# Kernel optimization log

Hardware: AMD Instinct MI355X
Metric: run time of the kernel (lower is better)

Reference implementation:

```python
import jax, jax.numpy as jnp
import numpy as np
import math

B, L, D = 4, 512, 768
H, DH, R = 12, 64, 128


def _layernorm(x, g, b, eps=1e-5):
    mu = jnp.mean(x, axis=-1, keepdims=True)
    var = jnp.var(x, axis=-1, keepdims=True)
    return (x - mu) * jax.lax.rsqrt(var + eps) * g + b


def setup_inputs() -> dict:
    key = jax.random.key(0)
    ks = jax.random.split(key, 8)
    s = 0.02
    return {
        "x": jax.random.normal(ks[0], (B, L, D), jnp.float32),
        "W_qkv": jax.random.normal(ks[1], (D, 3 * D), jnp.float32) * s,
        "b_qkv": jnp.zeros((3 * D,), jnp.float32),
        "W_b1": jax.random.normal(ks[2], (D, R), jnp.float32) * s,
        "W_b2": jax.random.normal(ks[3], (R, H * 5), jnp.float32) * s,
        "temperature": jnp.ones((1,), jnp.float32) * 0.5,
        "W_proj": jax.random.normal(ks[4], (D, D), jnp.float32) * s,
        "b_proj": jnp.zeros((D,), jnp.float32),
        "ln_g": jnp.ones((D,), jnp.float32),
        "ln_b": jnp.zeros((D,), jnp.float32),
        "mem_g": jnp.ones((DH,), jnp.float32),
        "mem_b": jnp.zeros((DH,), jnp.float32),
    }


def reference(x, W_qkv, b_qkv, W_b1, W_b2, temperature, W_proj, b_proj, ln_g, ln_b, mem_g, mem_b):
    Bq, Lq, Dq = x.shape
    xn = _layernorm(x, ln_g, ln_b)
    qkv = xn @ W_qkv + b_qkv
    q, k, v = jnp.split(qkv, 3, axis=-1)

    # bottleneck gating params: (B, L, H, 5)
    params = (jax.nn.silu(x @ W_b1) @ W_b2).reshape(Bq, Lq, H, 5)
    sem_amp = jax.nn.sigmoid(params[..., 0])
    sem_phase = jnp.tanh(params[..., 1]) * math.pi
    ctx_amp = jax.nn.sigmoid(params[..., 2])
    ctx_phase = jnp.tanh(params[..., 3]) * math.pi
    decay = 0.5 + 0.49 * jax.nn.sigmoid(params[..., 4])  # (B,L,H)

    temp = jnp.clip(temperature, 0.1, 2.0)  # (1,) broadcasts
    interference = jnp.tanh(sem_amp * ctx_amp * jnp.cos(sem_phase - ctx_phase)) * temp
    gate = jax.nn.sigmoid(interference)  # (B,L,H)

    qf = (jax.nn.elu(q) + 1.0).reshape(Bq, Lq, H, DH)
    kf = (jax.nn.elu(k) + 1.0).reshape(Bq, Lq, H, DH)
    vf = v.reshape(Bq, Lq, H, DH)

    log_decay = jnp.log(decay + 1e-8)
    cld = jnp.maximum(jnp.cumsum(log_decay, axis=1), -85.0)  # (B,L,H)
    df = jnp.exp(cld)
    inv_df = jnp.exp(-cld)
    ema = 1.0 - decay  # (B,L,H)

    # kv outer products gated by interference: (B,L,H,DH,DH)
    kv_all = jnp.einsum('blhd,blhe->blhde', kf, vf) * (1.0 + gate)[..., None, None]
    kv_states = jnp.cumsum(kv_all * (ema * inv_df)[..., None, None], axis=1) * df[..., None, None]

    z_states = jnp.cumsum(kf * (ema * inv_df)[..., None], axis=1) * df[..., None]  # (B,L,H,DH)

    out_num = jnp.einsum('blhd,blhde->blhe', qf, kv_states)
    den = jnp.sum(qf * z_states, axis=-1, keepdims=True) + 1e-6
    out = out_num / den  # (B,L,H,DH)

    out = _layernorm(out, mem_g, mem_b)
    attn_out = out.reshape(Bq, Lq, Dq)
    return attn_out @ W_proj + b_proj, gate
```

## Files before the change

### kernel.cpp

```cpp
#include <hip/hip_runtime.h>
#include <math.h>

#define PI_F 3.14159265358979323846f

static constexpr int L_ = 512, D_ = 768, H_ = 12, DH_ = 64;
static constexpr int BL_ = 2048;
static constexpr int BLD_ = BL_ * D_;
static constexpr int NC_ = 8;
static constexpr int BH_ = 48;

__global__ void sentinel_kernel(float* out, float code, float aux) {
  out[0] = code; out[1] = aux;
}

__global__ __launch_bounds__(256) void ln_kernel(const float* __restrict__ x,
                                                 const float* __restrict__ g,
                                                 const float* __restrict__ b,
                                                 float* __restrict__ xn) {
  int row = blockIdx.x, tid = threadIdx.x;
  const float* xr = x + (size_t)row * D_;
  float v0 = xr[tid], v1 = xr[tid + 256], v2 = xr[tid + 512];
  float s = v0 + v1 + v2;
  float s2 = v0 * v0 + v1 * v1 + v2 * v2;
#pragma unroll
  for (int off = 32; off > 0; off >>= 1) { s += __shfl_xor(s, off); s2 += __shfl_xor(s2, off); }
  __shared__ float red[8];
  if ((tid & 63) == 0) { red[tid >> 6] = s; red[4 + (tid >> 6)] = s2; }
  __syncthreads();
  float st = red[0] + red[1] + red[2] + red[3];
  float qt = red[4] + red[5] + red[6] + red[7];
  float mu = st * (1.0f / D_);
  float var = qt * (1.0f / D_) - mu * mu;
  float rs = rsqrtf(var + 1e-5f);
  float* xo = xn + (size_t)row * D_;
  xo[tid]       = (v0 - mu) * rs * g[tid]       + b[tid];
  xo[tid + 256] = (v1 - mu) * rs * g[tid + 256] + b[tid + 256];
  xo[tid + 512] = (v2 - mu) * rs * g[tid + 512] + b[tid + 512];
}

template <int MODE>
__global__ __launch_bounds__(256) void gemm_fast(const float* __restrict__ A,
                                                 const float* __restrict__ Bm,
                                                 const float* __restrict__ bias,
                                                 float* __restrict__ O0,
                                                 float* __restrict__ O1,
                                                 float* __restrict__ O2,
                                                 int N, int K) {
  __shared__ float As[16][68];
  __shared__ float Bs[16][68];
  int tid = threadIdx.x;
  int tx = tid & 15, ty = tid >> 4;
  int row0 = blockIdx.y * 64, col0 = blockIdx.x * 64;
  float acc[4][4] = {};
  int ar = tid >> 2, ak = (tid & 3) * 4;
  int bk = tid >> 4, bc = (tid & 15) * 4;
  for (int k0 = 0; k0 < K; k0 += 16) {
    float4 a4 = *(const float4*)&A[(size_t)(row0 + ar) * K + k0 + ak];
    As[ak + 0][ar] = a4.x; As[ak + 1][ar] = a4.y;
    As[ak + 2][ar] = a4.z; As[ak + 3][ar] = a4.w;
    *(float4*)&Bs[bk][bc] = *(const float4*)&Bm[(size_t)(k0 + bk) * N + col0 + bc];
    __syncthreads();
#pragma unroll
    for (int kk = 0; kk < 16; ++kk) {
      float4 av = *(float4*)&As[kk][ty * 4];
      float4 bv = *(float4*)&Bs[kk][tx * 4];
      acc[0][0] += av.x * bv.x; acc[0][1] += av.x * bv.y; acc[0][2] += av.x * bv.z; acc[0][3] += av.x * bv.w;
      acc[1][0] += av.y * bv.x; acc[1][1] += av.y * bv.y; acc[1][2] += av.y * bv.z; acc[1][3] += av.y * bv.w;
      acc[2][0] += av.z * bv.x; acc[2][1] += av.z * bv.y; acc[2][2] += av.z * bv.z; acc[2][3] += av.z * bv.w;
      acc[3][0] += av.w * bv.x; acc[3][1] += av.w * bv.y; acc[3][2] += av.w * bv.z; acc[3][3] += av.w * bv.w;
    }
    __syncthreads();
  }
  if (MODE == 0) {
    int sec = col0 / 768;
    float* O = (sec == 0) ? O0 : ((sec == 1) ? O1 : O2);
    int lc = col0 - sec * 768 + tx * 4;
    float b0 = bias[col0 + tx * 4 + 0], b1 = bias[col0 + tx * 4 + 1];
    float b2 = bias[col0 + tx * 4 + 2], b3 = bias[col0 + tx * 4 + 3];
#pragma unroll
    for (int ii = 0; ii < 4; ++ii) {
      int r = row0 + ty * 4 + ii;
      float4 v;
      v.x = acc[ii][0] + b0; v.y = acc[ii][1] + b1;
      v.z = acc[ii][2] + b2; v.w = acc[ii][3] + b3;
      if (sec < 2) {
        v.x = (v.x > 0.f) ? v.x + 1.f : expf(v.x);
        v.y = (v.y > 0.f) ? v.y + 1.f : expf(v.y);
        v.z = (v.z > 0.f) ? v.z + 1.f : expf(v.z);
        v.w = (v.w > 0.f) ? v.w + 1.f : expf(v.w);
      }
      *(float4*)&O[(size_t)r * 768 + lc] = v;
    }
  } else if (MODE == 1) {
#pragma unroll
    for (int ii = 0; ii < 4; ++ii) {
      int r = row0 + ty * 4 + ii;
      float4 v;
      v.x = acc[ii][0]; v.y = acc[ii][1]; v.z = acc[ii][2]; v.w = acc[ii][3];
      v.x = v.x / (1.f + expf(-v.x));
      v.y = v.y / (1.f + expf(-v.y));
      v.z = v.z / (1.f + expf(-v.z));
      v.w = v.w / (1.f + expf(-v.w));
      *(float4*)&O0[(size_t)r * N + col0 + tx * 4] = v;
    }
  } else {
    float b0 = bias[col0 + tx * 4 + 0], b1 = bias[col0 + tx * 4 + 1];
    float b2 = bias[col0 + tx * 4 + 2], b3 = bias[col0 + tx * 4 + 3];
#pragma unroll
    for (int ii = 0; ii < 4; ++ii) {
      int r = row0 + ty * 4 + ii;
      float4 v;
      v.x = acc[ii][0] + b0; v.y = acc[ii][1] + b1;
      v.z = acc[ii][2] + b2; v.w = acc[ii][3] + b3;
      *(float4*)&O0[(size_t)r * N + col0 + tx * 4] = v;
    }
  }
}

__global__ __launch_bounds__(64) void params_kernel(const float* __restrict__ h1,
                                                    const float* __restrict__ Wb2,
                                                    const float* __restrict__ temp_p,
                                                    float* __restrict__ gate_out,
                                                    float* __restrict__ cg,
                                                    float* __restrict__ ce,
                                                    float* __restrict__ ld) {
  int t = blockIdx.x;
  int tid = threadIdx.x;
  __shared__ float hs[128];
  __shared__ float ps[60];
  *(float2*)&hs[tid * 2] = *(const float2*)&h1[(size_t)t * 128 + tid * 2];
  __syncthreads();
  if (tid < 60) {
    float acc = 0.f;
#pragma unroll 4
    for (int k = 0; k < 128; ++k) acc += hs[k] * Wb2[k * 60 + tid];
    ps[tid] = acc;
  }
  __syncthreads();
  if (tid < 12) {
    float p0 = ps[tid * 5 + 0], p1 = ps[tid * 5 + 1], p2 = ps[tid * 5 + 2];
    float p3 = ps[tid * 5 + 3], p4 = ps[tid * 5 + 4];
    float sa = 1.f / (1.f + expf(-p0));
    float sp = tanhf(p1) * PI_F;
    float ca = 1.f / (1.f + expf(-p2));
    float cp = tanhf(p3) * PI_F;
    float dec = 0.5f + 0.49f / (1.f + expf(-p4));
    float tmp = fminf(fmaxf(temp_p[0], 0.1f), 2.0f);
    float inter = tanhf(sa * ca * cosf(sp - cp)) * tmp;
    float gate = 1.f / (1.f + expf(-inter));
    gate_out[t * 12 + tid] = gate;
    int b = t >> 9, l = t & 511;
    int bhl = (b * 12 + tid) * L_ + l;
    float ema = 1.f - dec;
    cg[bhl] = ema * (1.f + gate);
    ce[bhl] = ema;
    ld[bhl] = logf(dec + 1e-8f);
  }
}

__global__ __launch_bounds__(64) void cld_kernel(const float* __restrict__ ld,
                                                 float* __restrict__ cld,
                                                 float* __restrict__ cEnd) {
  int bh = blockIdx.x;
  int lane = threadIdx.x;
  const float* src = ld + (size_t)bh * L_;
  float v[8];
  float s = 0.f;
#pragma unroll
  for (int i = 0; i < 8; ++i) { v[i] = src[lane * 8 + i]; s += v[i]; }
  float tot = s;
#pragma unroll
  for (int off = 1; off < 64; off <<= 1) {
    float n = __shfl_up(tot, off);
    if (lane >= off) tot += n;
  }
  float run = tot - s;
  float out7 = 0.f;
#pragma unroll
  for (int i = 0; i < 8; ++i) {
    run += v[i];
    float o = fmaxf(run, -85.f);
    cld[(size_t)bh * L_ + lane * 8 + i] = o;
    out7 = o;
  }
  if ((lane & 7) == 7) cEnd[bh * NC_ + (lane >> 3)] = out7;
}

__global__ __launch_bounds__(64) void infscan_kernel(const float* __restrict__ kf,
                                                     const float* __restrict__ ce,
                                                     const float* __restrict__ cld,
                                                     int* __restrict__ tstar) {
  int bh = blockIdx.x;
  int b = bh / H_, h = bh - b * H_;
  int e = threadIdx.x;
  float cz = 0.f;
  int tf = L_;
  for (int t = 0; t < L_; ++t) {
    int idx = bh * L_ + t;
    float s = ce[idx] * expf(-cld[idx]);
    float kv = kf[(size_t)(b * L_ + t) * D_ + h * DH_ + e];
    cz = cz + kv * s;
    if (tf == L_ && isinf(cz)) tf = t;
  }
#pragma unroll
  for (int off = 1; off < 64; off <<= 1) tf = min(tf, __shfl_xor(tf, off));
  if (e == 0) tstar[bh] = tf;
}

__global__ __launch_bounds__(256) void chunk_sum_kernel(const float* __restrict__ kf,
                                                        const float* __restrict__ vf,
                                                        const float* __restrict__ cg,
                                                        const float* __restrict__ ce,
                                                        const float* __restrict__ cld,
                                                        const float* __restrict__ cEnd,
                                                        float* __restrict__ T,
                                                        float* __restrict__ zc) {
  int blk = blockIdx.x;
  int c = blk & 7, bh = blk >> 3;
  int b = bh / H_, h = bh - b * H_;
  int tid = threadIdx.x;
  __shared__ float kfs[64][68];
  __shared__ float vfs[64][68];
  __shared__ float wv[64], wz[64];
  float cend = cEnd[blk];
  if (tid < 64) {
    int idx = bh * L_ + c * 64 + tid;
    float w = expf(cend - cld[idx]);
    wv[tid] = cg[idx] * w;
    wz[tid] = ce[idx] * w;
  }
  __syncthreads();
  int t = tid >> 2, g4 = (tid & 3) * 16;
  size_t rowb = (size_t)(b * L_ + c * 64 + t) * D_ + h * 64 + g4;
  float wvt = wv[t];
#pragma unroll
  for (int i = 0; i < 4; ++i) {
    *(float4*)&kfs[t][g4 + 4 * i] = *(const float4*)&kf[rowb + 4 * i];
    float4 vv = *(const float4*)&vf[rowb + 4 * i];
    vv.x *= wvt; vv.y *= wvt; vv.z *= wvt; vv.w *= wvt;
    *(float4*)&vfs[t][g4 + 4 * i] = vv;
  }
  __syncthreads();
  int d = tid >> 2, eb = (tid & 3) * 16;
  float4 a0 = {}, a1 = {}, a2 = {}, a3 = {};
  for (int tt = 0; tt < 64; ++tt) {
    float kd = kfs[tt][d];
    float4 x0 = *(float4*)&vfs[tt][eb + 0];
    float4 x1 = *(float4*)&vfs[tt][eb + 4];
    float4 x2 = *(float4*)&vfs[tt][eb + 8];
    float4 x3 = *(float4*)&vfs[tt][eb + 12];
    a0.x += kd * x0.x; a0.y += kd * x0.y; a0.z += kd * x0.z; a0.w += kd * x0.w;
    a1.x += kd * x1.x; a1.y += kd * x1.y; a1.z += kd * x1.z; a1.w += kd * x1.w;
    a2.x += kd * x2.x; a2.y += kd * x2.y; a2.z += kd * x2.z; a2.w += kd * x2.w;
    a3.x += kd * x3.x; a3.y += kd * x3.y; a3.z += kd * x3.z; a3.w += kd * x3.w;
  }
  size_t tb = (size_t)blk * 4096 + (size_t)d * 64 + eb;
  *(float4*)&T[tb + 0] = a0;
  *(float4*)&T[tb + 4] = a1;
  *(float4*)&T[tb + 8] = a2;
  *(float4*)&T[tb + 12] = a3;
  if (tid < 64) {
    float za = 0.f;
#pragma unroll 8
    for (int tt = 0; tt < 64; ++tt) za += kfs[tt][tid] * wz[tt];
    zc[blk * 64 + tid] = za;
  }
}

__global__ __launch_bounds__(256) void scan_kernel(float* __restrict__ T,
                                                   const float* __restrict__ zc,
                                                   const float* __restrict__ cEnd,
                                                   float* __restrict__ zprev) {
  int bh = blockIdx.x, tid = threadIdx.x;
  float4 s0 = {}, s1 = {}, s2 = {}, s3 = {};
  float zs = 0.f;
  float prevEnd = 0.f;
  for (int c = 0; c < NC_; ++c) {
    int blk = bh * NC_ + c;
    float r = expf(cEnd[blk] - prevEnd);
    prevEnd = cEnd[blk];
    size_t base = (size_t)blk * 4096 + (size_t)tid * 16;
    float4 t0 = *(const float4*)&T[base + 0];
    float4 t1 = *(const float4*)&T[base + 4];
    float4 t2 = *(const float4*)&T[base + 8];
    float4 t3 = *(const float4*)&T[base + 12];
    *(float4*)&T[base + 0] = s0;
    *(float4*)&T[base + 4] = s1;
    *(float4*)&T[base + 8] = s2;
    *(float4*)&T[base + 12] = s3;
    s0.x = s0.x * r + t0.x; s0.y = s0.y * r + t0.y; s0.z = s0.z * r + t0.z; s0.w = s0.w * r + t0.w;
    s1.x = s1.x * r + t1.x; s1.y = s1.y * r + t1.y; s1.z = s1.z * r + t1.z; s1.w = s1.w * r + t1.w;
    s2.x = s2.x * r + t2.x; s2.y = s2.y * r + t2.y; s2.z = s2.z * r + t2.z; s2.w = s2.w * r + t2.w;
    s3.x = s3.x * r + t3.x; s3.y = s3.y * r + t3.y; s3.z = s3.z * r + t3.z; s3.w = s3.w * r + t3.w;
    if (tid < 64) {
      zprev[blk * 64 + tid] = zs;
      zs = zs * r + zc[blk * 64 + tid];
    }
  }
}

__global__ __launch_bounds__(256) void chunk_out_kernel(const float* __restrict__ qf,
                                                        const float* __restrict__ kf,
                                                        const float* __restrict__ vf,
                                                        const float* __restrict__ cg,
                                                        const float* __restrict__ ce,
                                                        const float* __restrict__ cld,
                                                        const float* __restrict__ cEnd,
                                                        const float* __restrict__ Sprev,
                                                        const float* __restrict__ zprev,
                                                        const int* __restrict__ tstar,
                                                        const float* __restrict__ mg,
                                                        const float* __restrict__ mb,
                                                        float* __restrict__ attn) {
  int blk = blockIdx.x;
  int c = blk & 7, bh = blk >> 3;
  int b = bh / H_, h = bh - b * H_;
  int tid = threadIdx.x;
  __shared__ float qfs[64][68];
  __shared__ float kfs[64][68];
  __shared__ float vfs[64][68];
  __shared__ float cldS[64], cgS[64], ceS[64], zS[64];
  int t = tid >> 2, g4 = (tid & 3) * 16;
  size_t rowb = (size_t)(b * L_ + c * 64 + t) * D_ + h * 64 + g4;
#pragma unroll
  for (int i = 0; i < 4; ++i) {
    *(float4*)&qfs[t][g4 + 4 * i] = *(const float4*)&qf[rowb + 4 * i];
    *(float4*)&kfs[t][g4 + 4 * i] = *(const float4*)&kf[rowb + 4 * i];
    *(float4*)&vfs[t][g4 + 4 * i] = *(const float4*)&vf[rowb + 4 * i];
  }
  if (tid < 64) {
    int idx = bh * L_ + c * 64 + tid;
    cldS[tid] = cld[idx];
    cgS[tid] = cg[idx];
    ceS[tid] = ce[idx];
    zS[tid] = zprev[blk * 64 + tid];
  }
  __syncthreads();
  float prevEnd = (c == 0) ? 0.f : cEnd[blk - 1];
  int ts = tstar[bh];
  int i = tid >> 2, jb = (tid & 3) * 16;
  float sc[16];
#pragma unroll
  for (int jj = 0; jj < 16; ++jj) sc[jj] = 0.f;
  for (int d = 0; d < 64; d += 4) {
    float4 q4 = *(float4*)&qfs[i][d];
#pragma unroll
    for (int jj = 0; jj < 16; ++jj) {
      float4 k4 = *(float4*)&kfs[jb + jj][d];
      sc[jj] += q4.x * k4.x + q4.y * k4.y + q4.z * k4.z + q4.w * k4.w;
    }
  }
  float cldi = cldS[i];
  float den = 0.f;
  float mvals[16];
#pragma unroll
  for (int jj = 0; jj < 16; ++jj) {
    int j = jb + jj;
    float w = (j <= i) ? expf(cldi - cldS[j]) : 0.f;
    float sw = sc[jj] * w;
    den += sw * ceS[j];
    mvals[jj] = sw * cgS[j];
  }
  float dz = 0.f;
#pragma unroll
  for (int dd = 0; dd < 16; ++dd) dz += qfs[i][jb + dd] * zS[jb + dd];
  den += __shfl_xor(den, 1); den += __shfl_xor(den, 2);
  dz += __shfl_xor(dz, 1);  dz += __shfl_xor(dz, 2);
  float wi = expf(cldi - prevEnd);
  den += wi * dz + 1e-6f;
  __syncthreads();
#pragma unroll
  for (int jj = 0; jj < 16; ++jj) kfs[i][jb + jj] = mvals[jj];
  __syncthreads();
  float4 o0 = {}, o1 = {}, o2 = {}, o3 = {};
  for (int j = 0; j < 64; ++j) {
    float m = kfs[i][j];
    float4 x0 = *(float4*)&vfs[j][jb + 0];
    float4 x1 = *(float4*)&vfs[j][jb + 4];
    float4 x2 = *(float4*)&vfs[j][jb + 8];
    float4 x3 = *(float4*)&vfs[j][jb + 12];
    o0.x += m * x0.x; o0.y += m * x0.y; o0.z += m * x0.z; o0.w += m * x0.w;
    o1.x += m * x1.x; o1.y += m * x1.y; o1.z += m * x1.z; o1.w += m * x1.w;
    o2.x += m * x2.x; o2.y += m * x2.y; o2.z += m * x2.z; o2.w += m * x2.w;
    o3.x += m * x3.x; o3.y += m * x3.y; o3.z += m * x3.z; o3.w += m * x3.w;
  }
  float4 p0 = {}, p1 = {}, p2 = {}, p3 = {};
  size_t sb = (size_t)blk * 4096;
  for (int d = 0; d < 64; ++d) {
    float qd = qfs[i][d];
    float4 x0 = *(const float4*)&Sprev[sb + d * 64 + jb + 0];
    float4 x1 = *(const float4*)&Sprev[sb + d * 64 + jb + 4];
    float4 x2 = *(const float4*)&Sprev[sb + d * 64 + jb + 8];
    float4 x3 = *(const float4*)&Sprev[sb + d * 64 + jb + 12];
    p0.x += qd * x0.x; p0.y += qd * x0.y; p0.z += qd * x0.z; p0.w += qd * x0.w;
    p1.x += qd * x1.x; p1.y += qd * x1.y; p1.z += qd * x1.z; p1.w += qd * x1.w;
    p2.x += qd * x2.x; p2.y += qd * x2.y; p2.z += qd * x2.z; p2.w += qd * x2.w;
    p3.x += qd * x3.x; p3.y += qd * x3.y; p3.z += qd * x3.z; p3.w += qd * x3.w;
  }
  size_t ob = (size_t)(b * L_ + c * 64 + i) * D_ + h * 64 + jb;
  if (c * 64 + i >= ts) {
#pragma unroll
    for (int q4i = 0; q4i < 4; ++q4i) {
      float4 w4;
      w4.x = mb[jb + q4i * 4 + 0]; w4.y = mb[jb + q4i * 4 + 1];
      w4.z = mb[jb + q4i * 4 + 2]; w4.w = mb[jb + q4i * 4 + 3];
      *(float4*)&attn[ob + q4i * 4] = w4;
    }
    return;
  }
  float inv = 1.0f / den;
  float o[16];
  o[0] = (o0.x + wi * p0.x) * inv;  o[1] = (o0.y + wi * p0.y) * inv;
  o[2] = (o0.z + wi * p0.z) * inv;  o[3] = (o0.w + wi * p0.w) * inv;
  o[4] = (o1.x + wi * p1.x) * inv;  o[5] = (o1.y + wi * p1.y) * inv;
  o[6] = (o1.z + wi * p1.z) * inv;  o[7] = (o1.w + wi * p1.w) * inv;
  o[8] = (o2.x + wi * p2.x) * inv;  o[9] = (o2.y + wi * p2.y) * inv;
  o[10] = (o2.z + wi * p2.z) * inv; o[11] = (o2.w + wi * p2.w) * inv;
  o[12] = (o3.x + wi * p3.x) * inv; o[13] = (o3.y + wi * p3.y) * inv;
  o[14] = (o3.z + wi * p3.z) * inv; o[15] = (o3.w + wi * p3.w) * inv;
  float s = 0.f, s2 = 0.f;
#pragma unroll
  for (int e2 = 0; e2 < 16; ++e2) { s += o[e2]; s2 += o[e2] * o[e2]; }
  s += __shfl_xor(s, 1);  s += __shfl_xor(s, 2);
  s2 += __shfl_xor(s2, 1); s2 += __shfl_xor(s2, 2);
  float mu = s * (1.f / 64.f);
  float var = s2 * (1.f / 64.f) - mu * mu;
  float rs = rsqrtf(var + 1e-5f);
#pragma unroll
  for (int q4i = 0; q4i < 4; ++q4i) {
    float4 w4;
    w4.x = (o[q4i * 4 + 0] - mu) * rs * mg[jb + q4i * 4 + 0] + mb[jb + q4i * 4 + 0];
    w4.y = (o[q4i * 4 + 1] - mu) * rs * mg[jb + q4i * 4 + 1] + mb[jb + q4i * 4 + 1];
    w4.z = (o[q4i * 4 + 2] - mu) * rs * mg[jb + q4i * 4 + 2] + mb[jb + q4i * 4 + 2];
    w4.w = (o[q4i * 4 + 3] - mu) * rs * mg[jb + q4i * 4 + 3] + mb[jb + q4i * 4 + 3];
    *(float4*)&attn[ob + q4i * 4] = w4;
  }
}

extern "C" void kernel_launch(void* const* d_in, const int* in_sizes, int n_in,
                              void* d_out, int out_size, void* d_ws, size_t ws_size,
                              hipStream_t stream) {
  const float* x     = (const float*)d_in[0];
  const float* Wqkv  = (const float*)d_in[1];
  const float* bqkv  = (const float*)d_in[2];
  const float* Wb1   = (const float*)d_in[3];
  const float* Wb2   = (const float*)d_in[4];
  const float* temp  = (const float*)d_in[5];
  const float* Wproj = (const float*)d_in[6];
  const float* bproj = (const float*)d_in[7];
  const float* lng   = (const float*)d_in[8];
  const float* lnb   = (const float*)d_in[9];
  const float* memg  = (const float*)d_in[10];
  const float* memb  = (const float*)d_in[11];
  float* out0 = (float*)d_out;
  float* gate = out0 + BLD_;

  static const int expect[12] = {1572864, 1769472, 2304, 98304, 7680, 1,
                                 589824, 768, 768, 768, 64, 64};
  int bad = (n_in == 12) ? -1 : 99;
  if (bad < 0) for (int i = 0; i < 12; ++i) if (in_sizes[i] != expect[i]) { bad = i; break; }
  size_t need = (size_t)(4 * BLD_ + 262144 + 4 * 24576) * sizeof(float);
  if (bad >= 0) { sentinel_kernel<<<1, 1, 0, stream>>>(out0, 3.0e6f, (float)bad); return; }
  if (ws_size < need) { sentinel_kernel<<<1, 1, 0, stream>>>(out0, 1.0e6f, (float)(ws_size >> 20)); return; }

  float* ws   = (float*)d_ws;
  float* xn   = ws;
  float* qfb  = xn + BLD_;
  float* kfb  = qfb + BLD_;
  float* vfb  = kfb + BLD_;
  float* h1   = vfb + BLD_;
  float* cgb  = h1 + 262144;
  float* ceb  = cgb + 24576;
  float* ldb  = ceb + 24576;
  float* cldb = ldb + 24576;
  float* Tb   = xn;
  float* zcb  = h1;
  float* zpv  = h1 + 24576;
  float* cEnd = h1 + 49152;
  int*   tstar = (int*)(h1 + 49536);
  float* attn = qfb;

  ln_kernel<<<BL_, 256, 0, stream>>>(x, lng, lnb, xn);
  gemm_fast<1><<<dim3(2, 32), 256, 0, stream>>>(x, Wb1, nullptr, h1, nullptr, nullptr, 128, 768);
  params_kernel<<<BL_, 64, 0, stream>>>(h1, Wb2, temp, gate, cgb, ceb, ldb);
  gemm_fast<0><<<dim3(36, 32), 256, 0, stream>>>(xn, Wqkv, bqkv, qfb, kfb, vfb, 2304, 768);
  cld_kernel<<<BH_, 64, 0, stream>>>(ldb, cldb, cEnd);
  infscan_kernel<<<BH_, 64, 0, stream>>>(kfb, ceb, cldb, tstar);
  chunk_sum_kernel<<<BH_ * NC_, 256, 0, stream>>>(kfb, vfb, cgb, ceb, cldb, cEnd, Tb, zcb);
  scan_kernel<<<BH_, 256, 0, stream>>>(Tb, zcb, cEnd, zpv);
  chunk_out_kernel<<<BH_ * NC_, 256, 0, stream>>>(qfb, kfb, vfb, cgb, ceb, cldb, cEnd,
                                                  Tb, zpv, tstar, memg, memb, attn);
  gemm_fast<2><<<dim3(12, 32), 256, 0, stream>>>(attn, Wproj, bproj, out0, nullptr, nullptr, 768, 768);
}
```

Baseline: 445.6 us.

## Fuse layernorm apply into QKV GEMM and enlarge GEMM row tiles

Layernorm now only computes per-row mean and rstd. The normalization is applied while loading A tiles inside the QKV GEMM, so the full normalized activation buffer is no longer written and read back. The QKV and output projection GEMMs move to a 128x64 tile with 8x4 outputs per thread, which gives more register reuse but halves the number of blocks (576 and 192). The cld kernel launch is also reordered ahead of the QKV GEMM.

```diff
diff --git a/kernel.cpp b/kernel.cpp
--- a/kernel.cpp
+++ b/kernel.cpp
@@ -13,10 +13,8 @@
   out[0] = code; out[1] = aux;
 }
 
-__global__ __launch_bounds__(256) void ln_kernel(const float* __restrict__ x,
-                                                 const float* __restrict__ g,
-                                                 const float* __restrict__ b,
-                                                 float* __restrict__ xn) {
+__global__ __launch_bounds__(256) void ln_stats(const float* __restrict__ x,
+                                                float* __restrict__ murs) {
   int row = blockIdx.x, tid = threadIdx.x;
   const float* xr = x + (size_t)row * D_;
   float v0 = xr[tid], v1 = xr[tid + 256], v2 = xr[tid + 512];
@@ -27,24 +25,114 @@
   __shared__ float red[8];
   if ((tid & 63) == 0) { red[tid >> 6] = s; red[4 + (tid >> 6)] = s2; }
   __syncthreads();
-  float st = red[0] + red[1] + red[2] + red[3];
-  float qt = red[4] + red[5] + red[6] + red[7];
-  float mu = st * (1.0f / D_);
-  float var = qt * (1.0f / D_) - mu * mu;
-  float rs = rsqrtf(var + 1e-5f);
-  float* xo = xn + (size_t)row * D_;
-  xo[tid]       = (v0 - mu) * rs * g[tid]       + b[tid];
-  xo[tid + 256] = (v1 - mu) * rs * g[tid + 256] + b[tid + 256];
-  xo[tid + 512] = (v2 - mu) * rs * g[tid + 512] + b[tid + 512];
+  if (tid == 0) {
+    float st = red[0] + red[1] + red[2] + red[3];
+    float qt = red[4] + red[5] + red[6] + red[7];
+    float mu = st * (1.0f / D_);
+    float var = qt * (1.0f / D_) - mu * mu;
+    murs[2 * row] = mu;
+    murs[2 * row + 1] = rsqrtf(var + 1e-5f);
+  }
 }
 
 template <int MODE>
-__global__ __launch_bounds__(256) void gemm_fast(const float* __restrict__ A,
+__global__ __launch_bounds__(256) void gemm_big(const float* __restrict__ A,
+                                                const float* __restrict__ murs,
+                                                const float* __restrict__ lg,
+                                                const float* __restrict__ lb,
+                                                const float* __restrict__ Bm,
+                                                const float* __restrict__ bias,
+                                                float* __restrict__ O0,
+                                                float* __restrict__ O1,
+                                                float* __restrict__ O2,
+                                                int N, int K) {
+  __shared__ float As[16][132];
+  __shared__ float Bs[16][68];
+  int tid = threadIdx.x;
+  int tx = tid & 15, ty = tid >> 4;
+  int row0 = blockIdx.y * 128, col0 = blockIdx.x * 64;
+  float acc[8][4] = {};
+  int ar = tid >> 1, ak = (tid & 1) * 8;
+  int bk = tid >> 4, bc = (tid & 15) * 4;
+  float mu = 0.f, rs = 0.f;
+  if (MODE == 0) {
+    float2 m2 = *(const float2*)&murs[2 * (row0 + ar)];
+    mu = m2.x; rs = m2.y;
+  }
+  const float* Arow = A + (size_t)(row0 + ar) * K;
+  for (int k0 = 0; k0 < K; k0 += 16) {
+    float4 a0 = *(const float4*)&Arow[k0 + ak];
+    float4 a1 = *(const float4*)&Arow[k0 + ak + 4];
+    if (MODE == 0) {
+      float4 g0 = *(const float4*)&lg[k0 + ak];
+      float4 g1 = *(const float4*)&lg[k0 + ak + 4];
+      float4 c0 = *(const float4*)&lb[k0 + ak];
+      float4 c1 = *(const float4*)&lb[k0 + ak + 4];
+      a0.x = (a0.x - mu) * rs * g0.x + c0.x;
+      a0.y = (a0.y - mu) * rs * g0.y + c0.y;
+      a0.z = (a0.z - mu) * rs * g0.z + c0.z;
+      a0.w = (a0.w - mu) * rs * g0.w + c0.w;
+      a1.x = (a1.x - mu) * rs * g1.x + c1.x;
+      a1.y = (a1.y - mu) * rs * g1.y + c1.y;
+      a1.z = (a1.z - mu) * rs * g1.z + c1.z;
+      a1.w = (a1.w - mu) * rs * g1.w + c1.w;
+    }
+    As[ak + 0][ar] = a0.x; As[ak + 1][ar] = a0.y;
+    As[ak + 2][ar] = a0.z; As[ak + 3][ar] = a0.w;
+    As[ak + 4][ar] = a1.x; As[ak + 5][ar] = a1.y;
+    As[ak + 6][ar] = a1.z; As[ak + 7][ar] = a1.w;
+    *(float4*)&Bs[bk][bc] = *(const float4*)&Bm[(size_t)(k0 + bk) * N + col0 + bc];
+    __syncthreads();
+#pragma unroll
+    for (int kk = 0; kk < 16; ++kk) {
+      float4 av0 = *(float4*)&As[kk][ty * 8];
+      float4 av1 = *(float4*)&As[kk][ty * 8 + 4];
+      float4 bv = *(float4*)&Bs[kk][tx * 4];
+      acc[0][0] += av0.x * bv.x; acc[0][1] += av0.x * bv.y; acc[0][2] += av0.x * bv.z; acc[0][3] += av0.x * bv.w;
+      acc[1][0] += av0.y * bv.x; acc[1][1] += av0.y * bv.y; acc[1][2] += av0.y * bv.z; acc[1][3] += av0.y * bv.w;
+      acc[2][0] += av0.z * bv.x; acc[2][1] += av0.z * bv.y; acc[2][2] += av0.z * bv.z; acc[2][3] += av0.z * bv.w;
+      acc[3][0] += av0.w * bv.x; acc[3][1] += av0.w * bv.y; acc[3][2] += av0.w * bv.z; acc[3][3] += av0.w * bv.w;
+      acc[4][0] += av1.x * bv.x; acc[4][1] += av1.x * bv.y; acc[4][2] += av1.x * bv.z; acc[4][3] += av1.x * bv.w;
+      acc[5][0] += av1.y * bv.x; acc[5][1] += av1.y * bv.y; acc[5][2] += av1.y * bv.z; acc[5][3] += av1.y * bv.w;
+      acc[6][0] += av1.z * bv.x; acc[6][1] += av1.z * bv.y; acc[6][2] += av1.z * bv.z; acc[6][3] += av1.z * bv.w;
+      acc[7][0] += av1.w * bv.x; acc[7][1] += av1.w * bv.y; acc[7][2] += av1.w * bv.z; acc[7][3] += av1.w * bv.w;
+    }
+    __syncthreads();
+  }
+  float4 bi = *(const float4*)&bias[col0 + tx * 4];
+  if (MODE == 0) {
+    int sec = col0 / 768;
+    float* O = (sec == 0) ? O0 : ((sec == 1) ? O1 : O2);
+    int lc = col0 - sec * 768 + tx * 4;
+#pragma unroll
+    for (int i = 0; i < 8; ++i) {
+      int r = row0 + ty * 8 + i;
+      float4 v;
+      v.x = acc[i][0] + bi.x; v.y = acc[i][1] + bi.y;
+      v.z = acc[i][2] + bi.z; v.w = acc[i][3] + bi.w;
+      if (sec < 2) {
+        v.x = (v.x > 0.f) ? v.x + 1.f : expf(v.x);
+        v.y = (v.y > 0.f) ? v.y + 1.f : expf(v.y);
+        v.z = (v.z > 0.f) ? v.z + 1.f : expf(v.z);
+        v.w = (v.w > 0.f) ? v.w + 1.f : expf(v.w);
+      }
+      *(float4*)&O[(size_t)r * 768 + lc] = v;
+    }
+  } else {
+#pragma unroll
+    for (int i = 0; i < 8; ++i) {
+      int r = row0 + ty * 8 + i;
+      float4 v;
+      v.x = acc[i][0] + bi.x; v.y = acc[i][1] + bi.y;
+      v.z = acc[i][2] + bi.z; v.w = acc[i][3] + bi.w;
+      *(float4*)&O0[(size_t)r * N + col0 + tx * 4] = v;
+    }
+  }
+}
+
+__global__ __launch_bounds__(256) void gemm_silu(const float* __restrict__ A,
                                                  const float* __restrict__ Bm,
-                                                 const float* __restrict__ bias,
                                                  float* __restrict__ O0,
-                                                 float* __restrict__ O1,
-                                                 float* __restrict__ O2,
                                                  int N, int K) {
   __shared__ float As[16][68];
   __shared__ float Bs[16][68];
@@ -71,49 +159,16 @@
     }
     __syncthreads();
   }
-  if (MODE == 0) {
-    int sec = col0 / 768;
-    float* O = (sec == 0) ? O0 : ((sec == 1) ? O1 : O2);
-    int lc = col0 - sec * 768 + tx * 4;
-    float b0 = bias[col0 + tx * 4 + 0], b1 = bias[col0 + tx * 4 + 1];
-    float b2 = bias[col0 + tx * 4 + 2], b3 = bias[col0 + tx * 4 + 3];
-#pragma unroll
-    for (int ii = 0; ii < 4; ++ii) {
-      int r = row0 + ty * 4 + ii;
-      float4 v;
-      v.x = acc[ii][0] + b0; v.y = acc[ii][1] + b1;
-      v.z = acc[ii][2] + b2; v.w = acc[ii][3] + b3;
-      if (sec < 2) {
-        v.x = (v.x > 0.f) ? v.x + 1.f : expf(v.x);
-        v.y = (v.y > 0.f) ? v.y + 1.f : expf(v.y);
-        v.z = (v.z > 0.f) ? v.z + 1.f : expf(v.z);
-        v.w = (v.w > 0.f) ? v.w + 1.f : expf(v.w);
-      }
-      *(float4*)&O[(size_t)r * 768 + lc] = v;
-    }
-  } else if (MODE == 1) {
-#pragma unroll
-    for (int ii = 0; ii < 4; ++ii) {
-      int r = row0 + ty * 4 + ii;
-      float4 v;
-      v.x = acc[ii][0]; v.y = acc[ii][1]; v.z = acc[ii][2]; v.w = acc[ii][3];
-      v.x = v.x / (1.f + expf(-v.x));
-      v.y = v.y / (1.f + expf(-v.y));
-      v.z = v.z / (1.f + expf(-v.z));
-      v.w = v.w / (1.f + expf(-v.w));
-      *(float4*)&O0[(size_t)r * N + col0 + tx * 4] = v;
-    }
-  } else {
-    float b0 = bias[col0 + tx * 4 + 0], b1 = bias[col0 + tx * 4 + 1];
-    float b2 = bias[col0 + tx * 4 + 2], b3 = bias[col0 + tx * 4 + 3];
-#pragma unroll
-    for (int ii = 0; ii < 4; ++ii) {
-      int r = row0 + ty * 4 + ii;
-      float4 v;
-      v.x = acc[ii][0] + b0; v.y = acc[ii][1] + b1;
-      v.z = acc[ii][2] + b2; v.w = acc[ii][3] + b3;
-      *(float4*)&O0[(size_t)r * N + col0 + tx * 4] = v;
-    }
+#pragma unroll
+  for (int ii = 0; ii < 4; ++ii) {
+    int r = row0 + ty * 4 + ii;
+    float4 v;
+    v.x = acc[ii][0]; v.y = acc[ii][1]; v.z = acc[ii][2]; v.w = acc[ii][3];
+    v.x = v.x / (1.f + expf(-v.x));
+    v.y = v.y / (1.f + expf(-v.y));
+    v.z = v.z / (1.f + expf(-v.z));
+    v.w = v.w / (1.f + expf(-v.w));
+    *(float4*)&O0[(size_t)r * N + col0 + tx * 4] = v;
   }
 }
 
@@ -473,6 +528,7 @@
   float* ceb  = cgb + 24576;
   float* ldb  = ceb + 24576;
   float* cldb = ldb + 24576;
+  float* murs = xn;
   float* Tb   = xn;
   float* zcb  = h1;
   float* zpv  = h1 + 24576;
@@ -480,15 +536,17 @@
   int*   tstar = (int*)(h1 + 49536);
   float* attn = qfb;
 
-  ln_kernel<<<BL_, 256, 0, stream>>>(x, lng, lnb, xn);
-  gemm_fast<1><<<dim3(2, 32), 256, 0, stream>>>(x, Wb1, nullptr, h1, nullptr, nullptr, 128, 768);
+  ln_stats<<<BL_, 256, 0, stream>>>(x, murs);
+  gemm_silu<<<dim3(2, 32), 256, 0, stream>>>(x, Wb1, h1, 128, 768);
   params_kernel<<<BL_, 64, 0, stream>>>(h1, Wb2, temp, gate, cgb, ceb, ldb);
-  gemm_fast<0><<<dim3(36, 32), 256, 0, stream>>>(xn, Wqkv, bqkv, qfb, kfb, vfb, 2304, 768);
   cld_kernel<<<BH_, 64, 0, stream>>>(ldb, cldb, cEnd);
+  gemm_big<0><<<dim3(36, 16), 256, 0, stream>>>(x, murs, lng, lnb, Wqkv, bqkv,
+                                                qfb, kfb, vfb, 2304, 768);
   infscan_kernel<<<BH_, 64, 0, stream>>>(kfb, ceb, cldb, tstar);
   chunk_sum_kernel<<<BH_ * NC_, 256, 0, stream>>>(kfb, vfb, cgb, ceb, cldb, cEnd, Tb, zcb);
   scan_kernel<<<BH_, 256, 0, stream>>>(Tb, zcb, cEnd, zpv);
   chunk_out_kernel<<<BH_ * NC_, 256, 0, stream>>>(qfb, kfb, vfb, cgb, ceb, cldb, cEnd,
                                                   Tb, zpv, tstar, memg, memb, attn);
-  gemm_fast<2><<<dim3(12, 32), 256, 0, stream>>>(attn, Wproj, bproj, out0, nullptr, nullptr, 768, 768);
-}
+  gemm_big<2><<<dim3(12, 16), 256, 0, stream>>>(attn, nullptr, nullptr, nullptr, Wproj,
+                                                bproj, out0, nullptr, nullptr, 768, 768);
+}
```

Measured after the change: 469.5 us. 1.05x slower.
